# Optimization experiments

Hardware: AMD Instinct MI355X
Metric: run time of the kernel (lower is better)

## Reference

```python
import jax, jax.numpy as jnp
import numpy as np

D = 256
H_GRID = 256
W_GRID = 256
N_LAYERS = 6


def _build_edges(H, W):
    # Vectorized equivalent of grid_to_graph's 4-neighbor edge construction.
    ii, jj = np.meshgrid(np.arange(H), np.arange(W), indexing='ij')
    srcs, dsts, feats = [], [], []
    for di, dj in [(-1, 0), (1, 0), (0, -1), (0, 1)]:
        ni, nj = ii + di, jj + dj
        m = (ni >= 0) & (ni < H) & (nj >= 0) & (nj < W)
        s = (ii * W + jj)[m]
        d = (ni * W + nj)[m]
        f = np.stack([
            np.full(s.shape, di, np.float32),
            np.full(s.shape, dj, np.float32),
            (ii[m] / H).astype(np.float32),
            (jj[m] / W).astype(np.float32),
        ], axis=-1)
        srcs.append(s); dsts.append(d); feats.append(f)
    edge_index = np.stack([np.concatenate(srcs), np.concatenate(dsts)]).astype(np.int32)
    edge_feats = np.concatenate(feats).astype(np.float32)
    return edge_index, edge_feats


def setup_inputs() -> dict:
    key = jax.random.key(0)
    ks = jax.random.split(key, 16)
    grid = jax.random.randint(ks[0], (H_GRID, W_GRID), 0, 10, dtype=jnp.int32)
    edge_index_np, edge_feats_np = _build_edges(H_GRID, W_GRID)
    edge_index = jnp.asarray(edge_index_np)
    edge_feats = jnp.asarray(edge_feats_np)

    def lin(k, fan_in, fan_out):
        bound = 1.0 / np.sqrt(fan_in)
        k1, k2 = jax.random.split(k)
        W = jax.random.uniform(k1, (fan_in, fan_out), jnp.float32, -bound, bound)
        b = jax.random.uniform(k2, (fan_out,), jnp.float32, -bound, bound)
        return W, b

    node_W, node_b = lin(ks[1], 1, D)

    def stack_lin(k, fan_in, fan_out):
        keys = jax.random.split(k, N_LAYERS)
        Ws, bs = zip(*[lin(kk, fan_in, fan_out) for kk in keys])
        return jnp.stack(Ws), jnp.stack(bs)

    msg_W1, msg_b1 = stack_lin(ks[2], 2 * D + 4, D)
    msg_W2, msg_b2 = stack_lin(ks[3], D, D)
    upd_W1, upd_b1 = stack_lin(ks[4], 2 * D, D)
    upd_W2, upd_b2 = stack_lin(ks[5], D, D)
    out_W, out_b = lin(ks[6], D, 10)

    return {
        'grid': grid, 'edge_index': edge_index, 'edge_feats': edge_feats,
        'node_W': node_W, 'node_b': node_b,
        'msg_W1': msg_W1, 'msg_b1': msg_b1, 'msg_W2': msg_W2, 'msg_b2': msg_b2,
        'upd_W1': upd_W1, 'upd_b1': upd_b1, 'upd_W2': upd_W2, 'upd_b2': upd_b2,
        'out_W': out_W, 'out_b': out_b,
    }


def reference(grid, edge_index, edge_feats, node_W, node_b,
              msg_W1, msg_b1, msg_W2, msg_b2,
              upd_W1, upd_b1, upd_W2, upd_b2,
              out_W, out_b):
    H, W = grid.shape
    N = H * W
    nodes = grid.astype(jnp.float32).reshape(N, 1)         # [N,1]
    h = nodes @ node_W + node_b                              # [N,D]
    src, tgt = edge_index[0], edge_index[1]

    def layer(h, params):
        mW1, mb1, mW2, mb2, uW1, ub1, uW2, ub2 = params
        # gather per-edge source/target features, run message MLP
        msg_in = jnp.concatenate([h[src], h[tgt], edge_feats], axis=-1)  # [E,2D+4]
        m = jax.nn.relu(msg_in @ mW1 + mb1) @ mW2 + mb2                   # [E,D]
        # scatter-add messages onto target nodes (vectorized segment sum)
        agg = jax.ops.segment_sum(m, tgt, num_segments=N)                 # [N,D]
        u_in = jnp.concatenate([h, agg], axis=-1)                         # [N,2D]
        h_new = jax.nn.relu(u_in @ uW1 + ub1) @ uW2 + ub2                 # [N,D]
        return h_new, None

    h, _ = jax.lax.scan(layer, h, (msg_W1, msg_b1, msg_W2, msg_b2,
                                   upd_W1, upd_b1, upd_W2, upd_b2))
    out = h @ out_W + out_b                                  # [N,10]
    return out.reshape(H, W, 10)
```

## Files before the change

### kernel.cpp

```cpp
#include <hip/hip_runtime.h>

#define HG 256
#define WGD 256
#define NN (HG*WGD)
#define NL 6

typedef _Float16 f16;
typedef _Float16 f16x8 __attribute__((ext_vector_type(8)));
typedef float f32x4 __attribute__((ext_vector_type(4)));

__device__ __forceinline__ void gload_lds16(const f16* g, f16* lds) {
  __builtin_amdgcn_global_load_lds(
      (const __attribute__((address_space(1))) unsigned int*)g,
      (__attribute__((address_space(3))) unsigned int*)lds, 16, 0, 0);
}

__global__ __launch_bounds__(256) void repack_frag(
    const f16* __restrict__ BtU, const f16* __restrict__ BtPQ,
    f16* __restrict__ BUf, f16* __restrict__ BPQf)
{
  int l = blockIdx.y, zz = blockIdx.z;
  int t = blockIdx.x*256 + threadIdx.x;
  int f = t >> 6;
  int lane = t & 63;
  if (zz == 0) {
    int NSs = (l==0) ? 8 : 16;
    if (f >= 16*NSs) return;
    int w2fn = f / NSs, ktks = f % NSs;
    int row = w2fn*16 + (lane & 15);
    int col = ktks*32 + (lane >> 4)*8;
    const f16* src = BtU + (size_t)l*131072 + ((l==0)?256:0) + (size_t)row*512 + col;
    *(f16x8*)(BUf + (size_t)l*131072 + (size_t)f*512 + lane*8) = *(const f16x8*)src;
  } else {
    if (l == 0) return;
    int ktks = f & 7, hw = f >> 3;
    int row = hw*16 + (lane & 15);
    int col = ktks*32 + (lane >> 4)*8;
    const f16* src = BtPQ + (size_t)l*131072 + (size_t)row*256 + col;
    *(f16x8*)(BPQf + (size_t)l*131072 + (size_t)f*512 + lane*8) = *(const f16x8*)src;
  }
}

template<int KK, int EPI, int DOPQ>
__global__ __launch_bounds__(512,4) void gemm_merge(
    const f16* __restrict__ A, int lda,
    const f16* __restrict__ BUf_,
    const f16* __restrict__ BPQf_,
    f16* __restrict__ Uo,
    f16* __restrict__ PQo,
    const float* __restrict__ bias,
    const float* __restrict__ v2,
    const float* __restrict__ avec,
    const int* __restrict__ gridv,
    const float* __restrict__ bias2)
{
  constexpr int NT = KK/64;
  constexpr int NSs = KK/32;
  __shared__ f16 sh[16384];
  const int tid  = threadIdx.x;
  const int lane = tid & 63;
  const int w    = tid >> 6;

  int bid = blockIdx.x;
  bid = (bid & 7) * 128 + (bid >> 3);
  const int mbase = bid * 64;

  f32x4 acc[4][2];
#pragma unroll
  for (int a=0;a<4;a++)
#pragma unroll
    for (int b=0;b<2;b++) acc[a][b] = (f32x4){0.f,0.f,0.f,0.f};

  const int r8  = lane >> 3;
  const int c8s = ((lane & 7) ^ r8) * 8;
  const f16* BUlane  = BUf_  + lane*8;
  const f16* BPQlane = (DOPQ ? BPQf_ : BUf_) + lane*8;

#define ASB(b) (sh + (b)*4096)
#define UL (sh)

#define STAGEA(kt, buf)                                                        \
  gload_lds16(A + (size_t)(mbase + w*8 + r8)*lda + (kt)*64 + c8s,              \
              ASB(buf) + w*512);

  f16x8 bfc[2][2];
#pragma unroll
  for (int ks=0; ks<2; ++ks)
#pragma unroll
    for (int fn=0; fn<2; ++fn)
      bfc[ks][fn] = *(const f16x8*)(BUlane + (size_t)((w*2+fn)*NSs + ks)*512);
  STAGEA(0, 0);
  __syncthreads();
  int cur = 0;
  for (int kt = 0; kt < NT; ++kt) {
    if (kt + 1 < NT) STAGEA(kt + 1, cur ^ 1);
    f16x8 bfn[2][2];
    if (kt + 1 < NT) {
#pragma unroll
      for (int ks=0; ks<2; ++ks)
#pragma unroll
        for (int fn=0; fn<2; ++fn)
          bfn[ks][fn] = *(const f16x8*)(BUlane +
                          (size_t)((w*2+fn)*NSs + (kt+1)*2+ks)*512);
    }
    const f16* Acur = ASB(cur);
#pragma unroll
    for (int ks=0; ks<2; ++ks) {
      const int off = (((ks*4 + (lane>>4)) ^ (lane & 7)) * 8);
      f16x8 af[4];
#pragma unroll
      for (int fm=0; fm<4; ++fm)
        af[fm] = *(const f16x8*)&Acur[(fm*16 + (lane&15))*64 + off];
#pragma unroll
      for (int fm=0; fm<4; ++fm)
#pragma unroll
        for (int fn=0; fn<2; ++fn)
          acc[fm][fn] = __builtin_amdgcn_mfma_f32_16x16x32_f16(af[fm], bfc[ks][fn], acc[fm][fn], 0,0,0);
    }
    __syncthreads();
#pragma unroll
    for (int ks=0; ks<2; ++ks)
#pragma unroll
      for (int fn=0; fn<2; ++fn)
        bfc[ks][fn] = bfn[ks][fn];
    cur ^= 1;
  }
#undef STAGEA

#pragma unroll
  for (int fm=0; fm<4; ++fm) {
#pragma unroll
    for (int fn=0; fn<2; ++fn) {
      const int coll = w*32 + fn*16 + (lane&15);
#pragma unroll
      for (int r=0;r<4;r++) {
        int rl  = fm*16 + (lane>>4)*4 + r;
        int row = mbase + rl;
        float v = acc[fm][fn][r];
        int i = row >> 8, j = row & 255;
        float deg = (float)((i>0)+(i<255)+(j>0)+(j<255));
        v += bias[coll] + deg * v2[coll];
        if (EPI==3) v += (float)gridv[row] * avec[coll];
        v = fmaxf(v, 0.f);
        f16 hv = (f16)v;
        Uo[(size_t)row*512 + coll] = hv;
        if (DOPQ) {
          int sblk = (coll >> 3) ^ (rl & 7);
          UL[rl*256 + sblk*8 + (coll & 7)] = hv;
        }
      }
    }
  }

  if (DOPQ) {
    __syncthreads();
#pragma unroll
    for (int h=0; h<2; ++h) {
      f32x4 acc2[4][2];
#pragma unroll
      for (int a=0;a<4;a++)
#pragma unroll
        for (int b=0;b<2;b++) acc2[a][b] = (f32x4){0.f,0.f,0.f,0.f};
#pragma unroll
      for (int kt=0; kt<4; ++kt) {
#pragma unroll
        for (int ks=0; ks<2; ++ks) {
          f16x8 af[4], bf[2];
#pragma unroll
          for (int fn=0; fn<2; ++fn)
            bf[fn] = *(const f16x8*)(BPQlane +
                       (size_t)(((h*16 + w*2+fn)*8) + kt*2+ks)*512);
#pragma unroll
          for (int fm=0; fm<4; ++fm) {
            int rl = fm*16 + (lane&15);
            int sblk = (kt*8 + ks*4 + (lane>>4)) ^ (rl & 7);
            af[fm] = *(const f16x8*)&UL[rl*256 + sblk*8];
          }
#pragma unroll
          for (int fm=0; fm<4; ++fm)
#pragma unroll
            for (int fn=0; fn<2; ++fn)
              acc2[fm][fn] = __builtin_amdgcn_mfma_f32_16x16x32_f16(af[fm], bf[fn], acc2[fm][fn], 0,0,0);
        }
      }
      const float* b2 = bias2 + h*256;
#pragma unroll
      for (int fm=0; fm<4; ++fm) {
#pragma unroll
        for (int fn=0; fn<2; ++fn) {
          const int coll = w*32 + fn*16 + (lane&15);
#pragma unroll
          for (int r=0;r<4;r++) {
            int row = mbase + fm*16 + (lane>>4)*4 + r;
            PQo[(size_t)row*512 + h*256 + coll] = (f16)(acc2[fm][fn][r] + b2[coll]);
          }
        }
      }
    }
  }
#undef UL
}

__device__ __forceinline__ void gemm_core256(
    const f16* __restrict__ A, int lda,
    const f16* __restrict__ Bt, int ldb,
    f16* __restrict__ C, int ldc,
    int mbase, int nbase, f16* As, f16* Bs)
{
  const int tid  = threadIdx.x;
  const int lane = tid & 63;
  const int w    = tid >> 6;
  const int wm   = w >> 1, wn = w & 1;

  f32x4 acc[4][4];
#pragma unroll
  for (int a=0;a<4;a++)
#pragma unroll
    for (int b=0;b<4;b++) acc[a][b] = (f32x4){0.f,0.f,0.f,0.f};

  const int r8  = lane >> 3;
  const int c8s = ((lane & 7) ^ r8) * 8;

  for (int kt = 0; kt < 4; ++kt) {
    const f16* Ab = A  + (size_t)(mbase + w*32)*lda + kt*64;
    const f16* Bb = Bt + (size_t)(nbase + w*32)*ldb + kt*64;
#pragma unroll
    for (int i=0;i<4;i++) {
      gload_lds16(Ab + (size_t)(i*8 + r8)*lda + c8s, &As[(w*32+i*8)*64]);
      gload_lds16(Bb + (size_t)(i*8 + r8)*ldb + c8s, &Bs[(w*32+i*8)*64]);
    }
    __syncthreads();
#pragma unroll
    for (int ks=0; ks<2; ++ks) {
      const int off = (((ks*4 + (lane>>4)) ^ (lane & 7)) * 8);
      f16x8 af[4], bf[4];
#pragma unroll
      for (int fm=0; fm<4; ++fm)
        af[fm] = *(const f16x8*)&As[(wm*64 + fm*16 + (lane&15))*64 + off];
#pragma unroll
      for (int fn=0; fn<4; ++fn)
        bf[fn] = *(const f16x8*)&Bs[(wn*64 + fn*16 + (lane&15))*64 + off];
#pragma unroll
      for (int fm=0; fm<4; ++fm)
#pragma unroll
        for (int fn=0; fn<4; ++fn)
          acc[fm][fn] = __builtin_amdgcn_mfma_f32_16x16x32_f16(af[fm], bf[fn], acc[fm][fn], 0,0,0);
    }
    __syncthreads();
  }

  const int row0 = mbase + wm*64 + (lane>>4)*4;
  const int col0 = nbase + wn*64 + (lane&15);
#pragma unroll
  for (int fm=0; fm<4; ++fm)
#pragma unroll
    for (int fn=0; fn<4; ++fn)
#pragma unroll
      for (int r=0;r<4;r++)
        C[(size_t)(row0 + fm*16 + r)*ldc + (col0 + fn*16)] = (f16)acc[fm][fn][r];
}

__global__ __launch_bounds__(256) void fold_all(
    const f16* __restrict__ BtA,  const f16* __restrict__ uW2h,
    const f16* __restrict__ mW2h, const f16* __restrict__ uW1aT,
    const f16* __restrict__ uW1bT,const f16* __restrict__ oWTh,
    f16* __restrict__ BtPQ, f16* __restrict__ BtU, f16* __restrict__ Wp2t)
{
  __shared__ f16 As[128*64];
  __shared__ f16 Bs[128*64];
  const int b = blockIdx.x;
  if (b < 40) {
    int z = b >> 3, rem = b & 7, x = rem & 3, y = rem >> 2;
    gemm_core256(BtA + (size_t)(z+1)*131072, 256, uW2h + (size_t)z*65536, 256,
                 BtPQ + (size_t)(z+1)*131072, 256, x*128, y*128, As, Bs);
  } else if (b < 60) {
    int rem = b - 40, z = rem >> 2, r2 = rem & 3, x = r2 & 1, y = r2 >> 1;
    gemm_core256(uW1aT + (size_t)(z+1)*65536, 256, uW2h + (size_t)z*65536, 256,
                 BtU + (size_t)(z+1)*131072, 512, x*128, y*128, As, Bs);
  } else if (b < 84) {
    int rem = b - 60, z = rem >> 2, r2 = rem & 3, x = r2 & 1, y = r2 >> 1;
    gemm_core256(uW1bT + (size_t)z*65536, 256, mW2h + (size_t)z*65536, 256,
                 BtU + (size_t)z*131072 + 256, 512, x*128, y*128, As, Bs);
  } else {
    int y = b - 84;
    gemm_core256(oWTh, 256, uW2h + (size_t)5*65536, 256,
                 Wp2t, 256, 0, y*128, As, Bs);
  }
}

template<int R1>
__global__ __launch_bounds__(256) void edge_fuse(
    const f16* __restrict__ PQ, f16* __restrict__ UR,
    const float* __restrict__ cvec, const float* __restrict__ wsi_,
    const float* __restrict__ wsj_,
    const int* __restrict__ gridv, const float* __restrict__ pa,
    const float* __restrict__ pc)
{
  const int t  = threadIdx.x;
  const int ln = t >> 5, ch = t & 31;
  int bid = blockIdx.x;
  bid = (bid & 7) * 1024 + (bid >> 3);
  const int n  = bid*8 + ln;
  const int i  = n >> 8, j = n & 255;
  const int co = ch*8;

  float q[8], pa0[8], pc0[8];
  if (R1) {
    float g = (float)gridv[n];
#pragma unroll
    for (int e=0;e<8;e++) {
      pa0[e] = pa[co+e]; pc0[e] = pc[co+e];
      q[e] = g*pa[256+co+e] + pc[256+co+e];
    }
  } else {
    f16x8 qv = *(const f16x8*)&PQ[(size_t)n*512 + 256 + co];
#pragma unroll
    for (int e=0;e<8;e++) q[e] = (float)qv[e];
  }
  float wi[8], wj[8];
#pragma unroll
  for (int e=0;e<8;e++){ wi[e]=wsi_[co+e]; wj[e]=wsj_[co+e]; }
  float acc[8];
#pragma unroll
  for (int e=0;e<8;e++) acc[e]=0.f;

  const int DI[4] = {-1,1,0,0};
  const int DJ[4] = {0,0,-1,1};
#pragma unroll
  for (int d=0; d<4; ++d) {
    int si = i - DI[d], sj = j - DJ[d];
    if (si>=0 && si<HG && sj>=0 && sj<WGD) {
      int s = si*WGD + sj;
      float fsi = si * (1.f/HG), fsj = sj * (1.f/WGD);
      float pvf[8];
      if (R1) {
        float gs = (float)gridv[s];
#pragma unroll
        for (int e=0;e<8;e++) pvf[e] = gs*pa0[e] + pc0[e];
      } else {
        f16x8 pv = *(const f16x8*)&PQ[(size_t)s*512 + co];
#pragma unroll
        for (int e=0;e<8;e++) pvf[e] = (float)pv[e];
      }
#pragma unroll
      for (int e=0;e<8;e++) {
        float v = pvf[e] + q[e] + cvec[d*256+co+e] + fsi*wi[e] + fsj*wj[e];
        acc[e] += fmaxf(v, 0.f);
      }
    }
  }
  f16x8 outv;
#pragma unroll
  for (int e=0;e<8;e++) outv[e] = (f16)acc[e];
  *(f16x8*)&UR[(size_t)n*512 + 256 + co] = outv;
}

__global__ __launch_bounds__(256) void out_mfma(
    const f16* __restrict__ U,
    const f16* __restrict__ Wp2t,
    const float* __restrict__ ob2,
    float* __restrict__ out)
{
  int lane = threadIdx.x & 63;
  int wv   = threadIdx.x >> 6;
  int nbase = blockIdx.x*64 + wv*16;
  f32x4 acc = (f32x4){0.f,0.f,0.f,0.f};
  int r  = lane & 15;
  int kg = (lane >> 4) * 8;
  const f16* Up = U + (size_t)(nbase + r)*512 + kg;
  const f16* Bp = Wp2t + r*256 + kg;
#pragma unroll
  for (int kt=0; kt<8; ++kt) {
    f16x8 af = *(const f16x8*)(Up + kt*32);
    f16x8 bf = *(const f16x8*)(Bp + kt*32);
    acc = __builtin_amdgcn_mfma_f32_16x16x32_f16(af, bf, acc, 0,0,0);
  }
  int col = lane & 15;
  int row0 = (lane>>4)*4;
  if (col < 10) {
    float bo = ob2[col];
#pragma unroll
    for (int rr=0; rr<4; ++rr)
      out[(size_t)(nbase + row0 + rr)*10 + col] = acc[rr] + bo;
  }
}

__global__ __launch_bounds__(256) void prep_small(
    const float* __restrict__ uW2, const float* __restrict__ mW2,
    const float* __restrict__ oW,  const float* __restrict__ mW1,
    const float* __restrict__ mb1, const float* __restrict__ mb2,
    const float* __restrict__ uW1, const float* __restrict__ ub1,
    const float* __restrict__ ub2, const float* __restrict__ nb,
    const float* __restrict__ nW,  const float* __restrict__ ob,
    f16* __restrict__ uW2h, f16* __restrict__ mW2h, f16* __restrict__ oWTh,
    float* __restrict__ cvec, float* __restrict__ wsi_, float* __restrict__ wsj_,
    float* __restrict__ v2, float* __restrict__ ubias, float* __restrict__ avec,
    float* __restrict__ pqb, float* __restrict__ pa, float* __restrict__ pc,
    float* __restrict__ ob2,
    f16* __restrict__ BtA, f16* __restrict__ uW1aT, f16* __restrict__ uW1bT)
{
  __shared__ float red[3][4][64];
  __shared__ float tbuf[32][33];
  const int b = blockIdx.x;
  const int tid = threadIdx.x;
  if (b < 1536) {
    int idx = b*256 + tid;
    uW2h[idx] = (f16)uW2[idx];
    mW2h[idx] = (f16)mW2[idx];
  } else if (b < 1664) {
    int c = b - 1536, j = tid;
    oWTh[c*256 + j] = (c < 10) ? (f16)oW[j*10 + c] : (f16)0.f;
  } else if (b < 1670) {
    int l = b - 1664, j = tid;
    const float* base = mW1 + (size_t)l*516*256;
    float w512 = base[512*256 + j], w513 = base[513*256 + j];
    float b1 = mb1[l*256 + j];
    const int DI[4] = {-1,1,0,0};
    const int DJ[4] = {0,0,-1,1};
    for (int d=0;d<4;d++)
      cvec[(l*4+d)*256 + j] = (float)DI[d]*w512 + (float)DJ[d]*w513 + b1;
    wsi_[l*256+j] = base[514*256 + j];
    wsj_[l*256+j] = base[515*256 + j];
  } else if (b < 1694) {
    int pr = tid & 63, q = tid >> 6;
    int pair = (b-1670)*64 + pr;
    int l = pair >> 8, j = pair & 255;
    const float* prevb = l ? (ub2 + (l-1)*256) : nb;
    float s1=0.f, s2=0.f, s3=0.f;
    for (int t = q*64; t < q*64+64; ++t) {
      s1 += mb2[l*256+t] * uW1[((size_t)l*512+256+t)*256 + j];
      s2 += prevb[t]     * uW1[((size_t)l*512+t)*256 + j];
      if (l==0) s3 += nW[t] * uW1[(size_t)t*256 + j];
    }
    red[0][q][pr]=s1; red[1][q][pr]=s2; red[2][q][pr]=s3;
    __syncthreads();
    if (q==0) {
      float a = red[0][0][pr]+red[0][1][pr]+red[0][2][pr]+red[0][3][pr];
      float bb = red[1][0][pr]+red[1][1][pr]+red[1][2][pr]+red[1][3][pr];
      v2[pair] = a;
      ubias[pair] = ub1[pair] + bb;
      if (l==0) avec[j] = red[2][0][pr]+red[2][1][pr]+red[2][2][pr]+red[2][3][pr];
    }
  } else if (b < 1742) {
    int pr = tid & 63, q = tid >> 6;
    int pair = (b-1694)*64 + pr;
    int l = pair >> 9, c = pair & 511;
    int rowoff = (c < 256) ? 0 : 256;
    int cc = c & 255;
    const float* base = mW1 + (size_t)l*516*256 + (size_t)rowoff*256 + cc;
    float s1=0.f, s2=0.f;
    if (l==0) {
      for (int j=q*64; j<q*64+64; ++j) { float wv = base[(size_t)j*256]; s1 += nW[j]*wv; s2 += nb[j]*wv; }
    } else {
      const float* pb = ub2 + (l-1)*256;
      for (int j=q*64; j<q*64+64; ++j) s1 += pb[j]*base[(size_t)j*256];
    }
    red[0][q][pr]=s1; red[1][q][pr]=s2;
    __syncthreads();
    if (q==0) {
      float a = red[0][0][pr]+red[0][1][pr]+red[0][2][pr]+red[0][3][pr];
      if (l==0) { pa[c]=a; pc[c]=red[1][0][pr]+red[1][1][pr]+red[1][2][pr]+red[1][3][pr]; }
      else pqb[pair] = a;
    }
  } else if (b == 1742) {
    int c = tid >> 4, jg = tid & 15;
    float s = 0.f;
    if (c < 10)
      for (int j=jg*16; j<jg*16+16; ++j) s += ub2[5*256+j]*oW[j*10+c];
    red[0][c>>2][(c&3)*16+jg] = s;
    __syncthreads();
    if (jg==0 && c < 16) {
      float a=0.f;
      for (int t2=0;t2<16;t2++) a += red[0][c>>2][(c&3)*16+t2];
      ob2[c] = (c < 10) ? a + ob[c] : 0.f;
    }
  } else {
    int t = b - 1743;
    int z = t >> 6, rem = t & 63;
    int bxs = (rem & 7) * 32, bys = (rem >> 3) * 32;
    const int q = z / 6, l = z % 6;
    const float* s;
    f16* d;
    if (q == 0)      { s = mW1 + (size_t)l*516*256;          d = BtA   + (size_t)l*131072; }
    else if (q == 1) { s = mW1 + (size_t)l*516*256 + 65536;  d = BtA   + (size_t)l*131072 + 65536; }
    else if (q == 2) { s = uW1 + (size_t)l*131072;           d = uW1aT + (size_t)l*65536; }
    else             { s = uW1 + (size_t)l*131072 + 65536;   d = uW1bT + (size_t)l*65536; }
    const int tx = tid & 31, ty = tid >> 5;
#pragma unroll
    for (int rr=0; rr<4; ++rr)
      tbuf[ty+rr*8][tx] = s[(size_t)(bys+ty+rr*8)*256 + bxs+tx];
    __syncthreads();
#pragma unroll
    for (int rr=0; rr<4; ++rr)
      d[(size_t)(bxs+ty+rr*8)*256 + bys+tx] = (f16)tbuf[tx][ty+rr*8];
  }
}

extern "C" void kernel_launch(void* const* d_in, const int* in_sizes, int n_in,
                              void* d_out, int out_size, void* d_ws, size_t ws_size,
                              hipStream_t stream)
{
  const int*   gridv = (const int*) d_in[0];
  const float* nW   = (const float*)d_in[3];
  const float* nb   = (const float*)d_in[4];
  const float* mW1  = (const float*)d_in[5];
  const float* mb1  = (const float*)d_in[6];
  const float* mW2  = (const float*)d_in[7];
  const float* mb2  = (const float*)d_in[8];
  const float* uW1  = (const float*)d_in[9];
  const float* ub1  = (const float*)d_in[10];
  const float* uW2  = (const float*)d_in[11];
  const float* ub2  = (const float*)d_in[12];
  const float* oW   = (const float*)d_in[13];
  const float* ob   = (const float*)d_in[14];
  float* out = (float*)d_out;

  char* ws = (char*)d_ws;
  size_t off = 0;
  f16* URa  = (f16*)(ws + off); off += (size_t)NN*512*2;
  f16* URb  = (f16*)(ws + off); off += (size_t)NN*512*2;
  f16* PQ   = (f16*)(ws + off); off += (size_t)NN*512*2;
  f16* BtA  = (f16*)(ws + off); off += 6*512*256*2;
  f16* BtPQ = (f16*)(ws + off); off += 6*512*256*2;
  f16* BtU  = (f16*)(ws + off); off += 6*256*512*2;
  f16* BUf  = (f16*)(ws + off); off += 6*131072*2;
  f16* BPQf = (f16*)(ws + off); off += 6*131072*2;
  f16* uW2h = (f16*)(ws + off); off += 6*256*256*2;
  f16* mW2h = (f16*)(ws + off); off += 6*256*256*2;
  f16* uW1aT= (f16*)(ws + off); off += 6*256*256*2;
  f16* uW1bT= (f16*)(ws + off); off += 6*256*256*2;
  f16* oWTh = (f16*)(ws + off); off += 128*256*2;
  f16* Wp2t = (f16*)(ws + off); off += 128*256*2;
  float* cvec = (float*)(ws + off); off += 6*4*256*4;
  float* wsi_ = (float*)(ws + off); off += 6*256*4;
  float* wsj_ = (float*)(ws + off); off += 6*256*4;
  float* v2   = (float*)(ws + off); off += 6*256*4;
  float* ubias= (float*)(ws + off); off += 6*256*4;
  float* pqb  = (float*)(ws + off); off += 6*512*4;
  float* pa   = (float*)(ws + off); off += 512*4;
  float* pc   = (float*)(ws + off); off += 512*4;
  float* avec = (float*)(ws + off); off += 256*4;
  float* ob2  = (float*)(ws + off); off += 16*4;

  prep_small<<<3279,256,0,stream>>>(uW2, mW2, oW, mW1, mb1, mb2, uW1, ub1, ub2,
                                    nb, nW, ob,
                                    uW2h, mW2h, oWTh, cvec, wsi_, wsj_,
                                    v2, ubias, avec, pqb, pa, pc, ob2,
                                    BtA, uW1aT, uW1bT);
  fold_all<<<86,256,0,stream>>>(BtA, uW2h, mW2h, uW1aT, uW1bT, oWTh,
                                BtPQ, BtU, Wp2t);
  repack_frag<<<dim3(64,6,2),256,0,stream>>>(BtU, BtPQ, BUf, BPQf);

  edge_fuse<1><<<8192,256,0,stream>>>(nullptr, URa, cvec, wsi_, wsj_, gridv, pa, pc);
  gemm_merge<256,3,1><<<1024,512,0,stream>>>(
      URa + 256, 512, BUf, BPQf + (size_t)1*131072,
      URb, PQ, ubias, v2, avec, gridv, pqb + 1*512);

  f16* cur = URb; f16* nxt = URa;
  for (int l=1;l<5;l++){
    edge_fuse<0><<<8192,256,0,stream>>>(PQ, cur, cvec + l*1024, wsi_ + l*256, wsj_ + l*256,
                                        nullptr, nullptr, nullptr);
    gemm_merge<512,1,1><<<1024,512,0,stream>>>(
        cur, 512, BUf + (size_t)l*131072, BPQf + (size_t)(l+1)*131072,
        nxt, PQ, ubias + l*256, v2 + l*256, nullptr, nullptr, pqb + (l+1)*512);
    f16* t = cur; cur = nxt; nxt = t;
  }

  edge_fuse<0><<<8192,256,0,stream>>>(PQ, cur, cvec + 5*1024, wsi_ + 5*256, wsj_ + 5*256,
                                      nullptr, nullptr, nullptr);
  gemm_merge<512,1,0><<<1024,512,0,stream>>>(
      cur, 512, BUf + (size_t)5*131072, nullptr,
      nxt, nullptr, ubias + 5*256, v2 + 5*256, nullptr, nullptr, nullptr);

  out_mfma<<<1024,256,0,stream>>>(nxt, Wp2t, ob2, out);
}
```

Before: 433.3 us.

## Fuse edge aggregation into gemm_merge prologue, staging aggregates directly into LDS

Removes the separate edge_fuse kernel. Each gemm_merge block now gathers neighbor PQ rows, computes the ReLU-summed messages for its 64 nodes in registers, and writes them straight into the LDS A-tile for the second half of K. The U buffer shrinks to 256 columns and PQ becomes double-buffered, because neighbor rows are read while other blocks write the next layer's PQ. This removes one launch per layer and the global write and re-read of the aggregate half of UR. In exchange the gather latency sits at the start of the GEMM without overlap, and register pressure rises under launch_bounds(512,4).

After: 871.5 us. +101.1%, slower.

```diff
diff --git a/kernel.cpp b/kernel.cpp
--- a/kernel.cpp
+++ b/kernel.cpp
@@ -44,6 +44,7 @@
 template<int KK, int EPI, int DOPQ>
 __global__ __launch_bounds__(512,4) void gemm_merge(
     const f16* __restrict__ A, int lda,
+    const f16* __restrict__ PQin,
     const f16* __restrict__ BUf_,
     const f16* __restrict__ BPQf_,
     f16* __restrict__ Uo,
@@ -52,7 +53,12 @@
     const float* __restrict__ v2,
     const float* __restrict__ avec,
     const int* __restrict__ gridv,
-    const float* __restrict__ bias2)
+    const float* __restrict__ bias2,
+    const float* __restrict__ cvecL,
+    const float* __restrict__ wsiL,
+    const float* __restrict__ wsjL,
+    const float* __restrict__ pa,
+    const float* __restrict__ pc)
 {
   constexpr int NT = KK/64;
   constexpr int NSs = KK/32;
@@ -76,12 +82,80 @@
   const f16* BUlane  = BUf_  + lane*8;
   const f16* BPQlane = (DOPQ ? BPQf_ : BUf_) + lane*8;
 
+  const int rT = tid >> 3;
+  const int cb = (tid & 7) * 32;
+  const int DIa[4] = {-1,1,0,0};
+  const int DJa[4] = {0,0,-1,1};
+  f16x8 rr[4];
+  {
+    const int n  = mbase + rT;
+    const int gi = n >> 8, gj = n & 255;
+    float gq = 0.f;
+    if (EPI==3) gq = (float)gridv[n];
+#pragma unroll
+    for (int e=0;e<4;++e){
+      const int ce = cb + e*8;
+      float q[8], a8[8];
+      if (EPI==3) {
+#pragma unroll
+        for (int k2=0;k2<8;k2++) q[k2] = gq*pa[256+ce+k2] + pc[256+ce+k2];
+      } else {
+        f16x8 qv = *(const f16x8*)&PQin[(size_t)n*512 + 256 + ce];
+#pragma unroll
+        for (int k2=0;k2<8;k2++) q[k2] = (float)qv[k2];
+      }
+#pragma unroll
+      for (int k2=0;k2<8;k2++) a8[k2]=0.f;
+#pragma unroll
+      for (int d=0; d<4; ++d) {
+        int si = gi - DIa[d], sj = gj - DJa[d];
+        if (si>=0 && si<HG && sj>=0 && sj<WGD) {
+          int sn = si*WGD + sj;
+          float fsi = si*(1.f/HG), fsj = sj*(1.f/WGD);
+          float pvf[8];
+          if (EPI==3) {
+            float gs = (float)gridv[sn];
+#pragma unroll
+            for (int k2=0;k2<8;k2++) pvf[k2] = gs*pa[ce+k2] + pc[ce+k2];
+          } else {
+            f16x8 pv = *(const f16x8*)&PQin[(size_t)sn*512 + ce];
+#pragma unroll
+            for (int k2=0;k2<8;k2++) pvf[k2] = (float)pv[k2];
+          }
+#pragma unroll
+          for (int k2=0;k2<8;k2++) {
+            float v = pvf[k2] + q[k2] + cvecL[d*256+ce+k2]
+                    + fsi*wsiL[ce+k2] + fsj*wsjL[ce+k2];
+            a8[k2] += fmaxf(v, 0.f);
+          }
+        }
+      }
+      f16x8 o;
+#pragma unroll
+      for (int k2=0;k2<8;k2++) o[k2] = (f16)a8[k2];
+      rr[e] = o;
+    }
+  }
+
 #define ASB(b) (sh + (b)*4096)
 #define UL (sh)
 
-#define STAGEA(kt, buf)                                                        \
-  gload_lds16(A + (size_t)(mbase + w*8 + r8)*lda + (kt)*64 + c8s,              \
-              ASB(buf) + w*512);
+#define STAGEC(kt_, buf_)                                                      \
+  { if (EPI!=3 && (kt_) < 4) {                                                 \
+      gload_lds16(A + (size_t)(mbase + w*8 + r8)*lda + (kt_)*64 + c8s,         \
+                  ASB(buf_) + w*512);                                          \
+    } else {                                                                   \
+      const int cch = (EPI==3) ? (kt_) : (kt_)-4;                              \
+      if (((tid & 7) >> 1) == cch) {                                           \
+        const int halfc = tid & 1;                                             \
+        _Pragma("unroll")                                                      \
+        for (int e=0;e<4;++e) {                                                \
+          int pb = (halfc*4 + e) ^ (rT & 7);                                   \
+          *(f16x8*)(ASB(buf_) + rT*64 + pb*8) = rr[e];                         \
+        }                                                                      \
+      }                                                                        \
+    }                                                                          \
+  }
 
   f16x8 bfc[2][2];
 #pragma unroll
@@ -89,11 +163,11 @@
 #pragma unroll
     for (int fn=0; fn<2; ++fn)
       bfc[ks][fn] = *(const f16x8*)(BUlane + (size_t)((w*2+fn)*NSs + ks)*512);
-  STAGEA(0, 0);
+  STAGEC(0, 0);
   __syncthreads();
   int cur = 0;
   for (int kt = 0; kt < NT; ++kt) {
-    if (kt + 1 < NT) STAGEA(kt + 1, cur ^ 1);
+    if (kt + 1 < NT) STAGEC(kt + 1, cur ^ 1);
     f16x8 bfn[2][2];
     if (kt + 1 < NT) {
 #pragma unroll
@@ -125,7 +199,7 @@
         bfc[ks][fn] = bfn[ks][fn];
     cur ^= 1;
   }
-#undef STAGEA
+#undef STAGEC
 
 #pragma unroll
   for (int fm=0; fm<4; ++fm) {
@@ -143,7 +217,7 @@
         if (EPI==3) v += (float)gridv[row] * avec[coll];
         v = fmaxf(v, 0.f);
         f16 hv = (f16)v;
-        Uo[(size_t)row*512 + coll] = hv;
+        Uo[(size_t)row*256 + coll] = hv;
         if (DOPQ) {
           int sblk = (coll >> 3) ^ (rl & 7);
           UL[rl*256 + sblk*8 + (coll & 7)] = hv;
@@ -199,6 +273,7 @@
     }
   }
 #undef UL
+#undef ASB
 }
 
 __device__ __forceinline__ void gemm_core256(
@@ -288,73 +363,6 @@
   }
 }
 
-template<int R1>
-__global__ __launch_bounds__(256) void edge_fuse(
-    const f16* __restrict__ PQ, f16* __restrict__ UR,
-    const float* __restrict__ cvec, const float* __restrict__ wsi_,
-    const float* __restrict__ wsj_,
-    const int* __restrict__ gridv, const float* __restrict__ pa,
-    const float* __restrict__ pc)
-{
-  const int t  = threadIdx.x;
-  const int ln = t >> 5, ch = t & 31;
-  int bid = blockIdx.x;
-  bid = (bid & 7) * 1024 + (bid >> 3);
-  const int n  = bid*8 + ln;
-  const int i  = n >> 8, j = n & 255;
-  const int co = ch*8;
-
-  float q[8], pa0[8], pc0[8];
-  if (R1) {
-    float g = (float)gridv[n];
-#pragma unroll
-    for (int e=0;e<8;e++) {
-      pa0[e] = pa[co+e]; pc0[e] = pc[co+e];
-      q[e] = g*pa[256+co+e] + pc[256+co+e];
-    }
-  } else {
-    f16x8 qv = *(const f16x8*)&PQ[(size_t)n*512 + 256 + co];
-#pragma unroll
-    for (int e=0;e<8;e++) q[e] = (float)qv[e];
-  }
-  float wi[8], wj[8];
-#pragma unroll
-  for (int e=0;e<8;e++){ wi[e]=wsi_[co+e]; wj[e]=wsj_[co+e]; }
-  float acc[8];
-#pragma unroll
-  for (int e=0;e<8;e++) acc[e]=0.f;
-
-  const int DI[4] = {-1,1,0,0};
-  const int DJ[4] = {0,0,-1,1};
-#pragma unroll
-  for (int d=0; d<4; ++d) {
-    int si = i - DI[d], sj = j - DJ[d];
-    if (si>=0 && si<HG && sj>=0 && sj<WGD) {
-      int s = si*WGD + sj;
-      float fsi = si * (1.f/HG), fsj = sj * (1.f/WGD);
-      float pvf[8];
-      if (R1) {
-        float gs = (float)gridv[s];
-#pragma unroll
-        for (int e=0;e<8;e++) pvf[e] = gs*pa0[e] + pc0[e];
-      } else {
-        f16x8 pv = *(const f16x8*)&PQ[(size_t)s*512 + co];
-#pragma unroll
-        for (int e=0;e<8;e++) pvf[e] = (float)pv[e];
-      }
-#pragma unroll
-      for (int e=0;e<8;e++) {
-        float v = pvf[e] + q[e] + cvec[d*256+co+e] + fsi*wi[e] + fsj*wj[e];
-        acc[e] += fmaxf(v, 0.f);
-      }
-    }
-  }
-  f16x8 outv;
-#pragma unroll
-  for (int e=0;e<8;e++) outv[e] = (f16)acc[e];
-  *(f16x8*)&UR[(size_t)n*512 + 256 + co] = outv;
-}
-
 __global__ __launch_bounds__(256) void out_mfma(
     const f16* __restrict__ U,
     const f16* __restrict__ Wp2t,
@@ -367,7 +375,7 @@
   f32x4 acc = (f32x4){0.f,0.f,0.f,0.f};
   int r  = lane & 15;
   int kg = (lane >> 4) * 8;
-  const f16* Up = U + (size_t)(nbase + r)*512 + kg;
+  const f16* Up = U + (size_t)(nbase + r)*256 + kg;
   const f16* Bp = Wp2t + r*256 + kg;
 #pragma unroll
   for (int kt=0; kt<8; ++kt) {
@@ -517,9 +525,9 @@
 
   char* ws = (char*)d_ws;
   size_t off = 0;
-  f16* URa  = (f16*)(ws + off); off += (size_t)NN*512*2;
-  f16* URb  = (f16*)(ws + off); off += (size_t)NN*512*2;
-  f16* PQ   = (f16*)(ws + off); off += (size_t)NN*512*2;
+  f16* Ust  = (f16*)(ws + off); off += (size_t)NN*256*2;
+  f16* PQa  = (f16*)(ws + off); off += (size_t)NN*512*2;
+  f16* PQb  = (f16*)(ws + off); off += (size_t)NN*512*2;
   f16* BtA  = (f16*)(ws + off); off += 6*512*256*2;
   f16* BtPQ = (f16*)(ws + off); off += 6*512*256*2;
   f16* BtU  = (f16*)(ws + off); off += 6*256*512*2;
@@ -551,26 +559,26 @@
                                 BtPQ, BtU, Wp2t);
   repack_frag<<<dim3(64,6,2),256,0,stream>>>(BtU, BtPQ, BUf, BPQf);
 
-  edge_fuse<1><<<8192,256,0,stream>>>(nullptr, URa, cvec, wsi_, wsj_, gridv, pa, pc);
   gemm_merge<256,3,1><<<1024,512,0,stream>>>(
-      URa + 256, 512, BUf, BPQf + (size_t)1*131072,
-      URb, PQ, ubias, v2, avec, gridv, pqb + 1*512);
-
-  f16* cur = URb; f16* nxt = URa;
+      nullptr, 256, nullptr, BUf, BPQf + (size_t)1*131072,
+      Ust, PQa, ubias, v2, avec, gridv, pqb + 1*512,
+      cvec, wsi_, wsj_, pa, pc);
+
+  f16* pin = PQa; f16* pout = PQb;
   for (int l=1;l<5;l++){
-    edge_fuse<0><<<8192,256,0,stream>>>(PQ, cur, cvec + l*1024, wsi_ + l*256, wsj_ + l*256,
-                                        nullptr, nullptr, nullptr);
     gemm_merge<512,1,1><<<1024,512,0,stream>>>(
-        cur, 512, BUf + (size_t)l*131072, BPQf + (size_t)(l+1)*131072,
-        nxt, PQ, ubias + l*256, v2 + l*256, nullptr, nullptr, pqb + (l+1)*512);
-    f16* t = cur; cur = nxt; nxt = t;
-  }
-
-  edge_fuse<0><<<8192,256,0,stream>>>(PQ, cur, cvec + 5*1024, wsi_ + 5*256, wsj_ + 5*256,
-                                      nullptr, nullptr, nullptr);
+        Ust, 256, pin, BUf + (size_t)l*131072, BPQf + (size_t)(l+1)*131072,
+        Ust, pout, ubias + l*256, v2 + l*256, nullptr, nullptr,
+        pqb + (l+1)*512, cvec + l*1024, wsi_ + l*256, wsj_ + l*256,
+        nullptr, nullptr);
+    f16* t = pin; pin = pout; pout = t;
+  }
+
   gemm_merge<512,1,0><<<1024,512,0,stream>>>(
-      cur, 512, BUf + (size_t)5*131072, nullptr,
-      nxt, nullptr, ubias + 5*256, v2 + 5*256, nullptr, nullptr, nullptr);
-
-  out_mfma<<<1024,256,0,stream>>>(nxt, Wp2t, ob2, out);
-}
+      Ust, 256, pin, BUf + (size_t)5*131072, nullptr,
+      Ust, nullptr, ubias + 5*256, v2 + 5*256, nullptr, nullptr,
+      nullptr, cvec + 5*1024, wsi_ + 5*256, wsj_ + 5*256,
+      nullptr, nullptr);
+
+  out_mfma<<<1024,256,0,stream>>>(Ust, Wp2t, ob2, out);
+}
```
